# Optimization experiments

Measured on AMD Instinct MI355X. Metric: run time of the kernel, lower is better.

The kernel has to match this reference:

```python
import jax, jax.numpy as jnp
import numpy as np

B, T, IN, H, OUT = 128, 512, 128, 1024, 64

def setup_inputs() -> dict:
    key = jax.random.key(0)
    ks = jax.random.split(key, 8)
    # xavier_normal with gain=0.5: std = 0.5*sqrt(2/(fan_in+fan_out))
    std_fiz = 0.5 * np.sqrt(2.0 / ((IN + H) + 3 * H))
    std_r = 0.5 * np.sqrt(2.0 / ((IN + H) + H))
    std_out = np.sqrt(1.0 / H)  # torch Linear default ~ uniform, normal ok for ref
    return {
        "u": jax.random.normal(ks[0], (B, T, IN), jnp.float32),
        "x0": jax.random.uniform(ks[1], (B, 1, 2 * H), jnp.float32),
        "kernel_fiz": jax.random.normal(ks[2], (IN + H, 3 * H), jnp.float32) * std_fiz,
        "bias_fiz": jnp.zeros((3 * H,), jnp.float32),
        "kernel_r": jax.random.normal(ks[3], (IN + H, H), jnp.float32) * std_r,
        "bias_r": jnp.zeros((H,), jnp.float32),
        "W_out": jax.random.normal(ks[4], (H, OUT), jnp.float32) * std_out,
        "b_out": jnp.zeros((OUT,), jnp.float32),
    }

def reference(u, x0, kernel_fiz, bias_fiz, kernel_r, bias_r, W_out, b_out):
    h0 = x0[:, 0, :H]   # [B, H]
    c0 = x0[:, 0, H:]   # [B, H]

    def step(carry, u_t):
        h, c = carry
        u_ = jnp.concatenate([u_t, h], axis=-1)          # [B, IN+H]
        fiz = jax.nn.sigmoid(u_ @ kernel_fiz + bias_fiz)  # [B, 3H]
        f, i, z = fiz[:, :H], fiz[:, H:2 * H], fiz[:, 2 * H:]
        r = jnp.tanh(u_ @ kernel_r + bias_r)              # [B, H]
        c_new = f * c + i * r
        h_new = z * jnp.tanh(c_new)
        y = h_new @ W_out + b_out                          # [B, OUT]
        return (h_new, c_new), y

    u_tbf = jnp.transpose(u, (1, 0, 2))  # [T, B, IN]
    _, y_tbf = jax.lax.scan(step, (h0, c0), u_tbf)
    return jnp.transpose(y_tbf, (1, 0, 2))  # [B, T, OUT]
```

## Files before the change

### kernel.cpp

```cpp
#include <hip/hip_runtime.h>
#include <hip/hip_bf16.h>

#define B_    128
#define T_    512
#define IN_   128
#define H_    1024
#define OUT_  64
#define KTOT  1152
#define GH    64
#define GB    4
#define HSLAB 131072
#define HBLK  2048

typedef short bf16x8 __attribute__((ext_vector_type(8)));
typedef float f32x4  __attribute__((ext_vector_type(4)));

#define MFMA(a,b,c) __builtin_amdgcn_mfma_f32_16x16x32_bf16((a),(b),(c),0,0,0)

__device__ __forceinline__ unsigned short f2bf(float x) {
    unsigned int xi = __float_as_uint(x);
    unsigned int r  = (xi + 0x7fffu + ((xi >> 16) & 1u)) >> 16;
    return (unsigned short)r;
}

__global__ void pack_weights(const float* __restrict__ kfiz, const float* __restrict__ kr,
                             const float* __restrict__ bfiz, const float* __restrict__ br,
                             unsigned short* __restrict__ Wp, float* __restrict__ biasp)
{
    const int c    = blockIdx.x;
    const int gh   = c >> 6, nl = c & 63;
    const int j    = gh * 16 + (nl >> 2);
    const int gate = nl & 3;
    for (int k = threadIdx.x; k < KTOT; k += 256) {
        float v = (gate < 3) ? kfiz[(size_t)k * 3072 + gate * 1024 + j]
                             : kr[(size_t)k * 1024 + j];
        Wp[(size_t)c * KTOT + k] = f2bf(v);
    }
    if (threadIdx.x == 0)
        biasp[c] = (gate < 3) ? bfiz[gate * 1024 + j] : br[j];
}

__global__ void pack_u(const float* __restrict__ u, unsigned short* __restrict__ Ubf)
{
    size_t i = (size_t)blockIdx.x * 256 + threadIdx.x;
    int t = (int)(i >> 14);
    int rem = (int)(i & 16383);
    int b = rem >> 7, k = rem & 127;
    Ubf[i] = f2bf(u[((size_t)b << 16) + ((size_t)t << 7) + k]);
}

__global__ void pack_wout(const float* __restrict__ wo, unsigned short* __restrict__ Wob)
{
    const int o = blockIdx.x;
    for (int k = threadIdx.x; k < H_; k += 256)
        Wob[(size_t)o * H_ + k] = f2bf(wo[(size_t)k * OUT_ + o]);
}

__global__ void __launch_bounds__(512, 2)
lstm_scan(const float* __restrict__ x0,
          const unsigned short* __restrict__ Wp,
          const float* __restrict__ biasp,
          const unsigned short* __restrict__ Ubf,
          unsigned short* __restrict__ Hall,
          int* __restrict__ Flag)
{
    __shared__ float part[4 * 8 * 320];
    __shared__ unsigned short hT[32 * 16];

    const int tid  = threadIdx.x;
    const int bid  = blockIdx.x;
    const int gb   = (bid & 7) >> 1;
    const int gh   = ((bid & 1) << 5) | (bid >> 3);
    const int wave = tid >> 6;
    const int lane = tid & 63;
    const int mi   = wave & 1;
    const int nj   = wave >> 1;
    const int quad = lane >> 4;
    const int l15  = lane & 15;
    const int g    = l15 & 3;

    f32x4 wregf[36];
    #pragma unroll
    for (int tl = 0; tl < 4; ++tl)
        #pragma unroll
        for (int kk = 0; kk < 9; ++kk)
            wregf[tl * 9 + kk] = *reinterpret_cast<const f32x4*>(
                Wp + (size_t)(gh * 64 + tl * 16 + l15) * KTOT + nj * 288 + kk * 32 + quad * 8);
    #pragma unroll
    for (int i = 0; i < 36; ++i)
        asm volatile("" : "+v"(wregf[i]));

    const float bias = biasp[gh * 64 + nj * 16 + l15];

    const int rowBase = gb * 32 + mi * 16;
    const int j       = gh * 16 + nj * 4 + (l15 >> 2);

    float cst[4];
    #pragma unroll
    for (int r = 0; r < 4; ++r)
        cst[r] = x0[(size_t)(rowBase + quad * 4 + r) * 2048 + 1024 + j];

    {
        int m = tid >> 4, uu = tid & 15;
        int b = gb * 32 + m;
        unsigned short hv = f2bf(x0[(size_t)b * 2048 + gh * 16 + uu]);
        __hip_atomic_store(&Hall[(size_t)gh * HBLK + (size_t)b * 16 + uu], hv,
                           __ATOMIC_RELAXED, __HIP_MEMORY_SCOPE_AGENT);
    }
    __syncthreads();
    if (tid == 0)
        __hip_atomic_store(&Flag[(size_t)gb * 64 + gh], 1,
                           __ATOMIC_RELAXED, __HIP_MEMORY_SCOPE_AGENT);

    const int aRow = rowBase + l15;
    const unsigned short* aU = Ubf + (size_t)aRow * IN_ + quad * 8;
    const unsigned short* aH = Hall + (size_t)aRow * 16 + (quad >> 1) * HBLK + (quad & 1) * 8;
    const ptrdiff_t hBlk0 = (ptrdiff_t)(nj * 18 - 8) * HBLK;

    const int kk0 = (nj == 0) ? 4 : 0;

    for (int t = 0; t < T_; ++t) {
        f32x4 acc[4] = {{0.f,0.f,0.f,0.f},{0.f,0.f,0.f,0.f},
                        {0.f,0.f,0.f,0.f},{0.f,0.f,0.f,0.f}};

        if (nj == 0) {
            const unsigned short* au = aU + (size_t)t * (B_ * IN_);
            #pragma unroll
            for (int kk = 0; kk < 4; ++kk) {
                bf16x8 av = *reinterpret_cast<const bf16x8*>(au + kk * 32);
                #pragma unroll
                for (int tl = 0; tl < 4; ++tl)
                    acc[tl] = MFMA(av, __builtin_bit_cast(bf16x8, wregf[tl * 9 + kk]), acc[tl]);
            }
        }

        if (wave == 0) {
            const int* fp = Flag + ((size_t)t * GB + gb) * 64 + lane;
            int v = __hip_atomic_load(fp, __ATOMIC_RELAXED, __HIP_MEMORY_SCOPE_AGENT);
            while (!__all(v != 0))
                v = __hip_atomic_load(fp, __ATOMIC_RELAXED, __HIP_MEMORY_SCOPE_AGENT);
        }
        __syncthreads();

        const ptrdiff_t hoff = (ptrdiff_t)t * HSLAB + hBlk0;
        bf16x8 a[9];
        #pragma unroll
        for (int kk = 0; kk < 9; ++kk)
            if (kk >= kk0)
                a[kk] = *reinterpret_cast<const bf16x8*>(aH + hoff + (ptrdiff_t)kk * (2 * HBLK));
        #pragma unroll
        for (int kk = 0; kk < 9; ++kk)
            if (kk >= kk0) {
                #pragma unroll
                for (int tl = 0; tl < 4; ++tl)
                    acc[tl] = MFMA(a[kk], __builtin_bit_cast(bf16x8, wregf[tl * 9 + kk]), acc[tl]);
            }

        #pragma unroll
        for (int tl = 0; tl < 4; ++tl)
            *reinterpret_cast<f32x4*>(
                &part[(nj * 8 + mi * 4 + tl) * 320 + l15 * 20 + quad * 4]) = acc[tl];
        __syncthreads();

        f32x4 s = {bias, bias, bias, bias};
        {
            const int rbase = (mi * 4 + nj) * 320 + l15 * 20 + quad * 4;
            #pragma unroll
            for (int njj = 0; njj < 4; ++njj)
                s += *reinterpret_cast<const f32x4*>(&part[njj * 2560 + rbase]);
        }

        #pragma unroll
        for (int r = 0; r < 4; ++r) {
            float pre = s[r];
            float sg  = 1.0f / (1.0f + __expf((g == 3) ? -2.0f * pre : -pre));
            float act = (g == 3) ? 2.0f * sg - 1.0f : sg;
            float x1 = __shfl_xor(act, 1);
            float x2 = __shfl_xor(act, 2);
            float x3 = __shfl_xor(x1, 2);
            float fv = (g == 0) ? act : (g == 1) ? x1 : (g == 2) ? x2 : x3;
            int gi = g ^ 1;
            float iv = (gi == 0) ? act : (gi == 1) ? x1 : (gi == 2) ? x2 : x3;
            int gz = g ^ 2;
            float zv = (gz == 0) ? act : (gz == 1) ? x1 : (gz == 2) ? x2 : x3;
            int gr = g ^ 3;
            float rv = (gr == 0) ? act : (gr == 1) ? x1 : (gr == 2) ? x2 : x3;

            float cn = fv * cst[r] + iv * rv;
            cst[r] = cn;
            float th = 2.0f / (1.0f + __expf(-2.0f * cn)) - 1.0f;
            float hn = zv * th;
            if (g == 0)
                hT[(mi * 16 + quad * 4 + r) * 16 + nj * 4 + (l15 >> 2)] = f2bf(hn);
        }

        __syncthreads();

        if (wave == 0) {
            const unsigned long long* lp =
                reinterpret_cast<const unsigned long long*>(hT);
            unsigned long long lo = lp[lane], hi = lp[lane + 64];
            size_t base = (size_t)(t + 1) * HSLAB + (size_t)gh * HBLK
                        + (size_t)(gb * 32) * 16;
            __hip_atomic_store((unsigned long long*)&Hall[base + lane * 4],       lo,
                               __ATOMIC_RELAXED, __HIP_MEMORY_SCOPE_AGENT);
            __hip_atomic_store((unsigned long long*)&Hall[base + 256 + lane * 4], hi,
                               __ATOMIC_RELAXED, __HIP_MEMORY_SCOPE_AGENT);
            __builtin_amdgcn_s_waitcnt(0);
            asm volatile("" ::: "memory");
            if (lane == 0)
                __hip_atomic_store(&Flag[((size_t)(t + 1) * GB + gb) * 64 + gh], 1,
                                   __ATOMIC_RELAXED, __HIP_MEMORY_SCOPE_AGENT);
        }
    }
}

__global__ void __launch_bounds__(256, 2)
out_gemm(const unsigned short* __restrict__ Hall,
         const unsigned short* __restrict__ Wob,
         const float* __restrict__ bout,
         float* __restrict__ y)
{
    const int tid  = threadIdx.x, wave = tid >> 6, lane = tid & 63;
    const int quad = lane >> 4, l15 = lane & 15;
    const int R    = blockIdx.x * 64 + wave * 16;

    f32x4 acc[4];
    #pragma unroll
    for (int nt = 0; nt < 4; ++nt) {
        float bb = bout[nt * 16 + l15];
        acc[nt] = {bb, bb, bb, bb};
    }
    const int fr = R + l15;
    const unsigned short* ap = Hall + ((size_t)(fr >> 7) + 1) * HSLAB
                             + (size_t)(fr & 127) * 16
                             + (quad >> 1) * HBLK + (quad & 1) * 8;
    #pragma unroll 4
    for (int kk = 0; kk < 32; ++kk) {
        bf16x8 av = *reinterpret_cast<const bf16x8*>(ap + (size_t)kk * (2 * HBLK));
        #pragma unroll
        for (int nt = 0; nt < 4; ++nt) {
            bf16x8 bv = *reinterpret_cast<const bf16x8*>(
                Wob + (size_t)(nt * 16 + l15) * H_ + kk * 32 + quad * 8);
            acc[nt] = MFMA(av, bv, acc[nt]);
        }
    }
    #pragma unroll
    for (int nt = 0; nt < 4; ++nt)
        #pragma unroll
        for (int r = 0; r < 4; ++r) {
            int row = R + quad * 4 + r;
            int b = row & 127, t = row >> 7;
            y[((size_t)b << 15) + ((size_t)t << 6) + nt * 16 + l15] = acc[nt][r];
        }
}

extern "C" void kernel_launch(void* const* d_in, const int* in_sizes, int n_in,
                              void* d_out, int out_size, void* d_ws, size_t ws_size,
                              hipStream_t stream)
{
    const float* u    = (const float*)d_in[0];
    const float* x0   = (const float*)d_in[1];
    const float* kfiz = (const float*)d_in[2];
    const float* bfiz = (const float*)d_in[3];
    const float* kr   = (const float*)d_in[4];
    const float* br   = (const float*)d_in[5];
    const float* wo   = (const float*)d_in[6];
    const float* bo   = (const float*)d_in[7];
    float* y = (float*)d_out;

    char* ws = (char*)d_ws;
    size_t off = 0;
    unsigned short* Wp    = (unsigned short*)(ws + off); off += (size_t)4096 * KTOT * 2;
    float*          biasp = (float*)(ws + off);          off += (size_t)4096 * 4;
    unsigned short* Wob   = (unsigned short*)(ws + off); off += (size_t)OUT_ * H_ * 2;
    unsigned short* Ubf   = (unsigned short*)(ws + off); off += (size_t)T_ * B_ * IN_ * 2;
    unsigned short* Hall  = (unsigned short*)(ws + off); off += (size_t)(T_ + 1) * B_ * H_ * 2;
    int*            Flag  = (int*)(ws + off);            off += (size_t)(T_ + 1) * GB * 64 * 4;
    if (off > ws_size) return;

    hipMemsetAsync(Flag, 0, (size_t)(T_ + 1) * GB * 64 * 4, stream);
    hipLaunchKernelGGL(pack_weights, dim3(4096),  dim3(256), 0, stream, kfiz, kr, bfiz, br, Wp, biasp);
    hipLaunchKernelGGL(pack_u,       dim3(32768), dim3(256), 0, stream, u, Ubf);
    hipLaunchKernelGGL(pack_wout,    dim3(64),    dim3(256), 0, stream, wo, Wob);

    void* args[] = { (void*)&x0, (void*)&Wp, (void*)&biasp, (void*)&Ubf, (void*)&Hall, (void*)&Flag };
    hipLaunchCooperativeKernel((void*)lstm_scan, dim3(GB * GH), dim3(512), args, 0, stream);

    hipLaunchKernelGGL(out_gemm, dim3((T_ * B_) / 64), dim3(256), 0, stream, Hall, Wob, bo, y);
}
```

Before: 2.061 ms.

## Replace flag barrier with per-wave sentinel polling on hidden-state data

The hidden-state buffer is pre-filled with 0xFFFF sentinels. Each wave now polls only the flags for the blocks it actually consumes, with a bounded spin, then re-reads its h operands with atomic loads until none of them holds the sentinel. This removes the block-wide __syncthreads after the flag wait and the producer's s_waitcnt before raising its flag, aiming to shorten the per-timestep cross-workgroup handoff. The cost is an extra memset of the whole Hall buffer, repeated operand reloads while spinning, and reliance on 0xFFFF never being a valid bf16 value (it is a NaN pattern). The bounded flag spin and the removed waitcnt may also weaken correctness guarantees.

```diff
diff --git a/kernel.cpp b/kernel.cpp
--- a/kernel.cpp
+++ b/kernel.cpp
@@ -14,6 +14,7 @@
 
 typedef short bf16x8 __attribute__((ext_vector_type(8)));
 typedef float f32x4  __attribute__((ext_vector_type(4)));
+typedef unsigned short u16x2 __attribute__((ext_vector_type(2)));
 
 #define MFMA(a,b,c) __builtin_amdgcn_mfma_f32_16x16x32_bf16((a),(b),(c),0,0,0)
 
@@ -119,6 +120,10 @@
 
     const int kk0 = (nj == 0) ? 4 : 0;
 
+    const int fBase = (nj == 0) ? 0 : (nj * 18 - 8);
+    const int fCnt  = (nj == 0) ? 10 : 18;
+    const int fl    = fBase + ((lane < fCnt) ? lane : (fCnt - 1));
+
     for (int t = 0; t < T_; ++t) {
         f32x4 acc[4] = {{0.f,0.f,0.f,0.f},{0.f,0.f,0.f,0.f},
                         {0.f,0.f,0.f,0.f},{0.f,0.f,0.f,0.f}};
@@ -134,26 +139,50 @@
             }
         }
 
-        if (wave == 0) {
-            const int* fp = Flag + ((size_t)t * GB + gb) * 64 + lane;
+        {
+            const int* fp = Flag + ((size_t)t * GB + gb) * 64 + fl;
             int v = __hip_atomic_load(fp, __ATOMIC_RELAXED, __HIP_MEMORY_SCOPE_AGENT);
-            while (!__all(v != 0))
+            int guard = 0;
+            while (!__all(v != 0) && guard < 262144) {
                 v = __hip_atomic_load(fp, __ATOMIC_RELAXED, __HIP_MEMORY_SCOPE_AGENT);
-        }
-        __syncthreads();
-
+                ++guard;
+            }
+        }
+
+        union AU { unsigned long long q[2]; bf16x8 v; } A[9];
         const ptrdiff_t hoff = (ptrdiff_t)t * HSLAB + hBlk0;
-        bf16x8 a[9];
-        #pragma unroll
-        for (int kk = 0; kk < 9; ++kk)
-            if (kk >= kk0)
-                a[kk] = *reinterpret_cast<const bf16x8*>(aH + hoff + (ptrdiff_t)kk * (2 * HBLK));
+        for (int spin = 0; spin < 4096; ++spin) {
+            u16x2 mx = (u16x2){0, 0};
+            #pragma unroll
+            for (int kk = 0; kk < 9; ++kk)
+                if (kk >= kk0) {
+                    const unsigned long long* gp =
+                        reinterpret_cast<const unsigned long long*>(
+                            aH + hoff + (ptrdiff_t)kk * (2 * HBLK));
+                    A[kk].q[0] = __hip_atomic_load(gp,     __ATOMIC_RELAXED, __HIP_MEMORY_SCOPE_AGENT);
+                    A[kk].q[1] = __hip_atomic_load(gp + 1, __ATOMIC_RELAXED, __HIP_MEMORY_SCOPE_AGENT);
+                }
+            #pragma unroll
+            for (int kk = 0; kk < 9; ++kk)
+                if (kk >= kk0) {
+                    #pragma unroll
+                    for (int hf = 0; hf < 2; ++hf) {
+                        unsigned long long q = A[kk].q[hf];
+                        mx = __builtin_elementwise_max(mx, __builtin_bit_cast(u16x2, (unsigned int)q));
+                        mx = __builtin_elementwise_max(mx, __builtin_bit_cast(u16x2, (unsigned int)(q >> 32)));
+                    }
+                }
+            bool ok = (mx.x != 0xFFFFu) && (mx.y != 0xFFFFu);
+            if (__all(ok)) break;
+            __builtin_amdgcn_s_sleep(1);
+        }
+
         #pragma unroll
         for (int kk = 0; kk < 9; ++kk)
             if (kk >= kk0) {
                 #pragma unroll
                 for (int tl = 0; tl < 4; ++tl)
-                    acc[tl] = MFMA(a[kk], __builtin_bit_cast(bf16x8, wregf[tl * 9 + kk]), acc[tl]);
+                    acc[tl] = MFMA(A[kk].v, __builtin_bit_cast(bf16x8, wregf[tl * 9 + kk]), acc[tl]);
             }
 
         #pragma unroll
@@ -206,7 +235,6 @@
                                __ATOMIC_RELAXED, __HIP_MEMORY_SCOPE_AGENT);
             __hip_atomic_store((unsigned long long*)&Hall[base + 256 + lane * 4], hi,
                                __ATOMIC_RELAXED, __HIP_MEMORY_SCOPE_AGENT);
-            __builtin_amdgcn_s_waitcnt(0);
             asm volatile("" ::: "memory");
             if (lane == 0)
                 __hip_atomic_store(&Flag[((size_t)(t + 1) * GB + gb) * 64 + gh], 1,
@@ -279,6 +307,7 @@
     int*            Flag  = (int*)(ws + off);            off += (size_t)(T_ + 1) * GB * 64 * 4;
     if (off > ws_size) return;
 
+    hipMemsetAsync(Hall, 0xFF, (size_t)(T_ + 1) * B_ * H_ * 2, stream);
     hipMemsetAsync(Flag, 0, (size_t)(T_ + 1) * GB * 64 * 4, stream);
     hipLaunchKernelGGL(pack_weights, dim3(4096),  dim3(256), 0, stream, kfiz, kr, bfiz, br, Wp, biasp);
     hipLaunchKernelGGL(pack_u,       dim3(32768), dim3(256), 0, stream, u, Ubf);
```

New measurement: 3.010 ms. 1.46x slower.

## Detect stale h data with 0xFFFF sentinel instead of waiting on store completion

Applied to the files above, without the earlier changes.

The h history buffer is prefilled with 0xFFFF so consumers can spot values that have not arrived yet. Each consumer validates its loaded h values and re-polls them with atomic loads until none hold the sentinel. This lets the producer drop its s_waitcnt before raising the flag, taking the store-drain latency off the per-step critical path. The cost is a large memset of the whole history buffer and extra compare work each step. The flag spin and the retry loop are now bounded, so a timeout silently falls through with possibly stale data, and the ordering between data and flag stores becomes weaker.

```diff
diff --git a/kernel.cpp b/kernel.cpp
--- a/kernel.cpp
+++ b/kernel.cpp
@@ -14,6 +14,8 @@
 
 typedef short bf16x8 __attribute__((ext_vector_type(8)));
 typedef float f32x4  __attribute__((ext_vector_type(4)));
+typedef unsigned int   u32x4 __attribute__((ext_vector_type(4)));
+typedef unsigned short u16x2 __attribute__((ext_vector_type(2)));
 
 #define MFMA(a,b,c) __builtin_amdgcn_mfma_f32_16x16x32_bf16((a),(b),(c),0,0,0)
 
@@ -137,7 +139,7 @@
         if (wave == 0) {
             const int* fp = Flag + ((size_t)t * GB + gb) * 64 + lane;
             int v = __hip_atomic_load(fp, __ATOMIC_RELAXED, __HIP_MEMORY_SCOPE_AGENT);
-            while (!__all(v != 0))
+            for (int guard = 0; guard < 16384 && !__all(v != 0); ++guard)
                 v = __hip_atomic_load(fp, __ATOMIC_RELAXED, __HIP_MEMORY_SCOPE_AGENT);
         }
         __syncthreads();
@@ -148,6 +150,43 @@
         for (int kk = 0; kk < 9; ++kk)
             if (kk >= kk0)
                 a[kk] = *reinterpret_cast<const bf16x8*>(aH + hoff + (ptrdiff_t)kk * (2 * HBLK));
+
+        {
+            u16x2 mx = (u16x2){0, 0};
+            #pragma unroll
+            for (int kk = 0; kk < 9; ++kk)
+                if (kk >= kk0) {
+                    u32x4 w = __builtin_bit_cast(u32x4, a[kk]);
+                    #pragma unroll
+                    for (int e = 0; e < 4; ++e)
+                        mx = __builtin_elementwise_max(mx, __builtin_bit_cast(u16x2, w[e]));
+                }
+            bool ok = (mx.x != 0xFFFFu) && (mx.y != 0xFFFFu);
+            if (!__all(ok)) {
+                for (int spin = 0; spin < 8192; ++spin) {
+                    union AU { unsigned long long q[2]; bf16x8 v; } tmp;
+                    u16x2 m2 = (u16x2){0, 0};
+                    #pragma unroll
+                    for (int kk = 0; kk < 9; ++kk)
+                        if (kk >= kk0) {
+                            const unsigned long long* gp =
+                                reinterpret_cast<const unsigned long long*>(
+                                    aH + hoff + (ptrdiff_t)kk * (2 * HBLK));
+                            tmp.q[0] = __hip_atomic_load(gp,     __ATOMIC_RELAXED, __HIP_MEMORY_SCOPE_AGENT);
+                            tmp.q[1] = __hip_atomic_load(gp + 1, __ATOMIC_RELAXED, __HIP_MEMORY_SCOPE_AGENT);
+                            a[kk] = tmp.v;
+                            u32x4 w = __builtin_bit_cast(u32x4, tmp.v);
+                            #pragma unroll
+                            for (int e = 0; e < 4; ++e)
+                                m2 = __builtin_elementwise_max(m2, __builtin_bit_cast(u16x2, w[e]));
+                        }
+                    bool ok2 = (m2.x != 0xFFFFu) && (m2.y != 0xFFFFu);
+                    if (__all(ok2)) break;
+                    __builtin_amdgcn_s_sleep(1);
+                }
+            }
+        }
+
         #pragma unroll
         for (int kk = 0; kk < 9; ++kk)
             if (kk >= kk0) {
@@ -206,7 +245,6 @@
                                __ATOMIC_RELAXED, __HIP_MEMORY_SCOPE_AGENT);
             __hip_atomic_store((unsigned long long*)&Hall[base + 256 + lane * 4], hi,
                                __ATOMIC_RELAXED, __HIP_MEMORY_SCOPE_AGENT);
-            __builtin_amdgcn_s_waitcnt(0);
             asm volatile("" ::: "memory");
             if (lane == 0)
                 __hip_atomic_store(&Flag[((size_t)(t + 1) * GB + gb) * 64 + gh], 1,
@@ -279,6 +317,7 @@
     int*            Flag  = (int*)(ws + off);            off += (size_t)(T_ + 1) * GB * 64 * 4;
     if (off > ws_size) return;
 
+    hipMemsetAsync(Hall, 0xFF, (size_t)(T_ + 1) * B_ * H_ * 2, stream);
     hipMemsetAsync(Flag, 0, (size_t)(T_ + 1) * GB * 64 * 4, stream);
     hipLaunchKernelGGL(pack_weights, dim3(4096),  dim3(256), 0, stream, kfiz, kr, bfiz, br, Wp, biasp);
     hipLaunchKernelGGL(pack_u,       dim3(32768), dim3(256), 0, stream, u, Ubf);
```

Result: slower. 2.921 ms (+41.8%).

## Release waves per K-slice as their producer flags arrive instead of block barrier

Applied to the files above, without the earlier changes.

Replaces the per-step block-wide __syncthreads after flag polling with fine-grained release. Wave 0 polls the 64 producer flags and publishes a per-nj LDS release counter as soon as the subset of producers covering that wave group's K-range is ready. Other waves spin on their own counter, so each group can start its MFMAs early instead of waiting for the slowest producer. This adds LDS spin traffic and bounded loops that could time out silently, and removes a barrier that may have protected shared-buffer reuse.

```diff
diff --git a/kernel.cpp b/kernel.cpp
--- a/kernel.cpp
+++ b/kernel.cpp
@@ -66,6 +66,7 @@
 {
     __shared__ float part[4 * 8 * 320];
     __shared__ unsigned short hT[32 * 16];
+    __shared__ int rel[4];
 
     const int tid  = threadIdx.x;
     const int bid  = blockIdx.x;
@@ -100,6 +101,8 @@
     for (int r = 0; r < 4; ++r)
         cst[r] = x0[(size_t)(rowBase + quad * 4 + r) * 2048 + 1024 + j];
 
+    if (tid < 4) rel[tid] = 0;
+
     {
         int m = tid >> 4, uu = tid & 15;
         int b = gb * 32 + m;
@@ -136,11 +139,36 @@
 
         if (wave == 0) {
             const int* fp = Flag + ((size_t)t * GB + gb) * 64 + lane;
-            int v = __hip_atomic_load(fp, __ATOMIC_RELAXED, __HIP_MEMORY_SCOPE_AGENT);
-            while (!__all(v != 0))
-                v = __hip_atomic_load(fp, __ATOMIC_RELAXED, __HIP_MEMORY_SCOPE_AGENT);
-        }
-        __syncthreads();
+            int relMask = 0;
+            for (int gd = 0; gd < (1 << 16); ++gd) {
+                int v = __hip_atomic_load(fp, __ATOMIC_RELAXED, __HIP_MEMORY_SCOPE_AGENT);
+                unsigned long long b = __ballot(v != 0);
+                if (lane == 0) {
+                    if (!(relMask & 1) && (b & 0x3FFull) == 0x3FFull) {
+                        __hip_atomic_store(&rel[0], t + 1, __ATOMIC_RELEASE, __HIP_MEMORY_SCOPE_WORKGROUP);
+                        relMask |= 1;
+                    }
+                    if (!(relMask & 2) && (b & 0x0FFFFC00ull) == 0x0FFFFC00ull) {
+                        __hip_atomic_store(&rel[1], t + 1, __ATOMIC_RELEASE, __HIP_MEMORY_SCOPE_WORKGROUP);
+                        relMask |= 2;
+                    }
+                    if (!(relMask & 4) && (b & 0x00003FFFF0000000ull) == 0x00003FFFF0000000ull) {
+                        __hip_atomic_store(&rel[2], t + 1, __ATOMIC_RELEASE, __HIP_MEMORY_SCOPE_WORKGROUP);
+                        relMask |= 4;
+                    }
+                    if (!(relMask & 8) && (b & 0xFFFFC00000000000ull) == 0xFFFFC00000000000ull) {
+                        __hip_atomic_store(&rel[3], t + 1, __ATOMIC_RELEASE, __HIP_MEMORY_SCOPE_WORKGROUP);
+                        relMask |= 8;
+                    }
+                }
+                if (b == ~0ull) break;
+            }
+        } else {
+            for (int gd = 0; gd < (1 << 18); ++gd)
+                if (__hip_atomic_load(&rel[nj], __ATOMIC_ACQUIRE, __HIP_MEMORY_SCOPE_WORKGROUP) >= t + 1)
+                    break;
+        }
+        asm volatile("" ::: "memory");
 
         const ptrdiff_t hoff = (ptrdiff_t)t * HSLAB + hBlk0;
         bf16x8 a[9];
```

After: 2.159 ms. +4.8%, slower.
